# Kernel tuning notes

Measured on AMD Instinct MI355X. Metric: run time of the kernel, lower is better.

The kernel has to match this reference:

```python
import jax, jax.numpy as jnp
import numpy as np

N_IN, M_MID = 512, 256
B, H, W = 16, 64, 64

def setup_inputs() -> dict:
    key = jax.random.key(0)
    ks = jax.random.split(key, 7)
    s = 0.05
    return {
        "x": jax.random.normal(ks[0], (B, N_IN, H, W), dtype=jnp.float32),
        "W_state": jax.random.normal(ks[1], (M_MID, N_IN), dtype=jnp.float32) * s,
        "b_state": jax.random.normal(ks[2], (M_MID,), dtype=jnp.float32) * s,
        "W_proj": jax.random.normal(ks[3], (M_MID, N_IN), dtype=jnp.float32) * s,
        "b_proj": jax.random.normal(ks[4], (M_MID,), dtype=jnp.float32) * s,
        "W_extend": jax.random.normal(ks[5], (N_IN, M_MID), dtype=jnp.float32) * s,
        "b_extend": jax.random.normal(ks[6], (N_IN,), dtype=jnp.float32) * s,
    }

def reference(x, W_state, b_state, W_proj, b_proj, W_extend, b_extend):
    n, c, h, w = x.shape
    hw = h * w
    xf = x.reshape(n, c, hw)                                   # [n, C, HW]
    # 1x1 convs are channel GEMMs over flattened spatial dim
    x_state = jnp.einsum('mc,nch->nmh', W_state, xf) + b_state[None, :, None]   # [n, M, HW]
    x_proj = jnp.einsum('mc,nch->nmh', W_proj, xf) + b_proj[None, :, None]      # [n, M, HW]
    # bmm -> scale -> softmax -> bmm (graph reasoning over M x M)
    scores = jnp.einsum('nmh,nkh->nmk', x_state, x_proj) / jnp.sqrt(jnp.float32(hw))
    attn = jax.nn.softmax(scores, axis=2)                      # [n, M, M]
    x_rstate = jnp.einsum('nmk,nkh->nmh', attn, x_proj)        # [n, M, HW]
    # extend back to C channels + residual
    ext = jnp.einsum('cm,nmh->nch', W_extend, x_rstate) + b_extend[None, :, None]
    return x + ext.reshape(n, c, h, w)
```

## Files before the change

kernel.cpp:

```cpp
#include <hip/hip_runtime.h>
#include <hip/hip_bf16.h>
#include <stdint.h>

typedef __bf16 bf16x8_t __attribute__((ext_vector_type(8)));
typedef float  f32x4_t  __attribute__((ext_vector_type(4)));
typedef short  short8_t __attribute__((ext_vector_type(8)));

__device__ __forceinline__ unsigned short f2b(float f) {
    union { float f; unsigned u; } v; v.f = f;
    unsigned u = v.u;
    return (unsigned short)((u + 0x7FFFu + ((u >> 16) & 1u)) >> 16);
}
__device__ __forceinline__ float b2f(unsigned short b) {
    union { unsigned u; float f; } v; v.u = ((unsigned)b) << 16; return v.f;
}

#define AS3(p) ((__attribute__((address_space(3))) void*)(p))
#define AS1(p) ((const __attribute__((address_space(1))) void*)(p))
#define FENCE() asm volatile("" ::: "memory")

#define NB   16
#define CIN  512
#define MMID 256
#define HW   4096
#define KSPLIT 8
#define ASZ  (128 * 64)

__device__ __forceinline__ void swz3(int gx, int gy, int& bx, int& by, int& bz) {
    const int nwg = gridDim.x, ord = blockIdx.x, q = nwg >> 3;
    const int s = (ord & 7) * q + (ord >> 3);
    by = s % gy;
    const int rem = s / gy;
    bx = rem % gx;
    bz = rem / gx;
}

__global__ __launch_bounds__(256) void prep_weights(
    const float* __restrict__ Ws, const float* __restrict__ Wp,
    const float* __restrict__ Wef, const float* __restrict__ bs,
    const float* __restrict__ bp,
    unsigned short* __restrict__ Wsp, unsigned short* __restrict__ Wex,
    unsigned short* __restrict__ WpT, float* __restrict__ bsp)
{
    int i = blockIdx.x * 256 + threadIdx.x;
    if (i < MMID * CIN) {
        Wsp[i]              = f2b(Ws[i]);
        Wsp[MMID * CIN + i] = f2b(Wp[i]);
        Wex[i]              = f2b(Wef[i]);
        const int c = i >> 8, k = i & (MMID - 1);
        WpT[i] = f2b(Wp[(size_t)k * CIN + c]);
    }
    if (i < MMID) { bsp[i] = bs[i]; bsp[MMID + i] = bp[i]; }
}

__global__ __launch_bounds__(256) void transpose_convert_x(
    const float* __restrict__ x, unsigned short* __restrict__ xT)
{
    __shared__ unsigned short tile[64][66];
    const int n = blockIdx.z, c0 = blockIdx.y * 64, h0 = blockIdx.x * 64;
    const float* s = x + ((size_t)n * CIN + c0) * HW + h0;
    unsigned short* d = xT + ((size_t)n * HW + h0) * CIN + c0;
    const int t = threadIdx.x;
    {
        const int rr = t >> 4, cc = (t & 15) * 4;
        #pragma unroll
        for (int p = 0; p < 4; ++p) {
            int r = p * 16 + rr;
            float4 v = *(const float4*)(s + (size_t)r * HW + cc);
            tile[r][cc + 0] = f2b(v.x); tile[r][cc + 1] = f2b(v.y);
            tile[r][cc + 2] = f2b(v.z); tile[r][cc + 3] = f2b(v.w);
        }
    }
    __syncthreads();
    {
        const int wr = t >> 3, wc = (t & 7) * 8;
        #pragma unroll
        for (int p = 0; p < 2; ++p) {
            int h = p * 32 + wr;
            unsigned short tmp[8];
            #pragma unroll
            for (int j = 0; j < 8; ++j) tmp[j] = tile[wc + j][h];
            *(short8_t*)(d + (size_t)h * CIN + wc) = *(const short8_t*)tmp;
        }
    }
}

__global__ __launch_bounds__(256) void transpose_bf16_64(
    const unsigned short* __restrict__ src, unsigned short* __restrict__ dst,
    int srs, int drs, long long sbs, long long dbs)
{
    __shared__ unsigned short tile[64][66];
    const int n = blockIdx.z, r0 = blockIdx.y * 64, c0 = blockIdx.x * 64;
    const unsigned short* s = src + (size_t)n * sbs + (size_t)r0 * srs + c0;
    unsigned short* d = dst + (size_t)n * dbs + (size_t)c0 * drs + r0;
    const int t = threadIdx.x;
    const int rr = t >> 3, cc = (t & 7) * 8;
    #pragma unroll
    for (int p = 0; p < 2; ++p) {
        int r = p * 32 + rr;
        short8_t v = *(const short8_t*)(s + (size_t)r * srs + cc);
        #pragma unroll
        for (int j = 0; j < 8; ++j) tile[r][cc + j] = ((const unsigned short*)&v)[j];
    }
    __syncthreads();
    #pragma unroll
    for (int p = 0; p < 2; ++p) {
        int c = p * 32 + rr;
        unsigned short tmp[8];
        #pragma unroll
        for (int j = 0; j < 8; ++j) tmp[j] = tile[cc + j][c];
        *(short8_t*)(d + (size_t)c * drs + cc) = *(const short8_t*)tmp;
    }
}

template <int EPI>
__device__ __forceinline__ void epilogue_repack(
    f32x4_t (&acc)[4][4], unsigned short* smem,
    int m0, int n0, int wave, int lane,
    const float* __restrict__ bias, const float* __restrict__ resid,
    void* __restrict__ Cout, int ldc, size_t cbase)
{
    float* fbuf = (float*)smem;
    const int t   = wave * 64 + lane;
    const int l15 = lane & 15, l16 = lane >> 4;
    const int wr2 = wave >> 1;
    const int wc  = (wave & 1) * 64;

    #pragma unroll
    for (int p = 0; p < 4; ++p) {
        __syncthreads();
        if (wr2 == (p >> 1)) {
            const int ihalf = p & 1;
            #pragma unroll
            for (int i2 = 0; i2 < 2; ++i2) {
                const int i = ihalf * 2 + i2;
                #pragma unroll
                for (int r = 0; r < 4; ++r) {
                    const int lrow = i2 * 16 + l16 * 4 + r;
                    #pragma unroll
                    for (int j = 0; j < 4; ++j)
                        fbuf[lrow * 132 + wc + j * 16 + l15] = acc[i][j][r];
                }
            }
        }
        __syncthreads();
        #pragma unroll
        for (int it = 0; it < 2; ++it) {
            const int lrow = it * 16 + (t >> 4);
            const int col  = (t & 15) * 8;
            const int row  = m0 + p * 32 + lrow;
            float v[8];
            *(float4*)&v[0] = *(const float4*)&fbuf[lrow * 132 + col];
            *(float4*)&v[4] = *(const float4*)&fbuf[lrow * 132 + col + 4];
            float badd = 0.f;
            if constexpr (EPI == 0 || EPI == 3) badd = bias[row];
            const size_t idx = cbase + (size_t)row * ldc + n0 + col;
            if constexpr (EPI == 3) {
                float o[8];
                const float* rp = resid + idx;
                float4 r0 = *(const float4*)rp;
                float4 r1 = *(const float4*)(rp + 4);
                o[0] = v[0] + badd + r0.x; o[1] = v[1] + badd + r0.y;
                o[2] = v[2] + badd + r0.z; o[3] = v[3] + badd + r0.w;
                o[4] = v[4] + badd + r1.x; o[5] = v[5] + badd + r1.y;
                o[6] = v[6] + badd + r1.z; o[7] = v[7] + badd + r1.w;
                float* op = (float*)Cout + idx;
                *(float4*)op = *(const float4*)&o[0];
                *(float4*)(op + 4) = *(const float4*)&o[4];
            } else if constexpr (EPI == 1) {
                float* op = (float*)Cout + idx;
                *(float4*)op = *(const float4*)&v[0];
                *(float4*)(op + 4) = *(const float4*)&v[4];
            } else {
                unsigned short o[8];
                #pragma unroll
                for (int k = 0; k < 8; ++k) o[k] = f2b(v[k] + badd);
                *(short8_t*)((unsigned short*)Cout + idx) = *(const short8_t*)o;
            }
        }
    }
}

#define GEMM_KLOOP(Ab, Bb, lda, ldb, KBEG, NT)                                          \
    auto stage = [&](int k0, int b) {                                                   \
        unsigned short* Asb = smem + b * 2 * ASZ;                                       \
        unsigned short* Bsb = Asb + ASZ;                                                \
        _Pragma("unroll")                                                               \
        for (int c = 0; c < 4; ++c) {                                                   \
            const int o   = (c * 256 + t) * 16;                                         \
            const int row = o >> 7;                                                     \
            const int ce  = ((o & 127) ^ ((row & 7) << 4)) >> 1;                        \
            __builtin_amdgcn_global_load_lds(                                           \
                AS1(Ab + (size_t)row * lda + k0 + ce), AS3((char*)Asb + o), 16, 0, 0);  \
            __builtin_amdgcn_global_load_lds(                                           \
                AS1(Bb + (size_t)row * ldb + k0 + ce), AS3((char*)Bsb + o), 16, 0, 0);  \
        }                                                                               \
    };                                                                                  \
    stage(KBEG, 0);                                                                     \
    for (int itk = 0; itk < (NT); ++itk) {                                              \
        const int cur = itk & 1;                                                        \
        if (itk + 1 < (NT)) {                                                           \
            stage(KBEG + (itk + 1) * 64, cur ^ 1);                                      \
            asm volatile("s_waitcnt vmcnt(8)" ::: "memory");                            \
        } else {                                                                        \
            asm volatile("s_waitcnt vmcnt(0)" ::: "memory");                            \
        }                                                                               \
        __builtin_amdgcn_s_barrier();                                                   \
        FENCE();                                                                        \
        const char* Asb = (const char*)(smem + cur * 2 * ASZ);                          \
        const char* Bsb = Asb + 2 * ASZ;                                                \
        const int swz = (l15 & 7) << 4;                                                 \
        _Pragma("unroll")                                                               \
        for (int ks = 0; ks < 2; ++ks) {                                                \
            bf16x8_t af[4], bfr[4];                                                     \
            const int cb = (ks * 64 + l16 * 16) ^ swz;                                  \
            _Pragma("unroll")                                                           \
            for (int i = 0; i < 4; ++i) {                                               \
                af[i]  = *(const bf16x8_t*)(Asb + (wr + i * 16 + l15) * 128 + cb);      \
                bfr[i] = *(const bf16x8_t*)(Bsb + (wc + i * 16 + l15) * 128 + cb);      \
            }                                                                           \
            _Pragma("unroll")                                                           \
            for (int i = 0; i < 4; ++i)                                                 \
                _Pragma("unroll")                                                       \
                for (int j = 0; j < 4; ++j)                                             \
                    acc[i][j] = __builtin_amdgcn_mfma_f32_16x16x32_bf16(                \
                        af[i], bfr[j], acc[i][j], 0, 0, 0);                             \
        }                                                                               \
        FENCE();                                                                        \
        __builtin_amdgcn_s_barrier();                                                   \
        FENCE();                                                                        \
    }

__global__ __launch_bounds__(256) void gemm_conv(
    const unsigned short* __restrict__ Wsp, const unsigned short* __restrict__ xT,
    const float* __restrict__ bsp, unsigned short* __restrict__ Ysp)
{
    __shared__ unsigned short smem[4 * ASZ];

    int bx, by, n;  swz3(HW / 128, CIN / 128, bx, by, n);
    const int m0 = by * 128;
    const int h0 = bx * 128;

    const unsigned short* Ab = Wsp + (size_t)m0 * CIN;
    const unsigned short* Bb = xT + (size_t)n * HW * CIN + (size_t)h0 * CIN;

    const int t    = threadIdx.x;
    const int lane = t & 63;
    const int wave = t >> 6;
    const int wr   = (wave >> 1) * 64;
    const int wc   = (wave & 1) * 64;
    const int l15  = lane & 15;
    const int l16  = lane >> 4;

    f32x4_t acc[4][4] = {};
    GEMM_KLOOP(Ab, Bb, CIN, CIN, 0, CIN / 64)

    epilogue_repack<0>(acc, smem, m0, h0, wave, lane, bsp, nullptr,
                       Ysp, HW, (size_t)n * CIN * HW);
}

__global__ __launch_bounds__(256) void gemm_scores(
    const unsigned short* __restrict__ Ysp, float* __restrict__ scoresP)
{
    __shared__ unsigned short smem[4 * ASZ];

    int bx, by, z;  swz3(MMID / 128, MMID / 128, bx, by, z);
    const int n  = z >> 3;
    const int kc = z & 7;
    const int m0 = by * 128;
    const int n0 = bx * 128;

    const unsigned short* Ab = Ysp + (size_t)n * CIN * HW + (size_t)m0 * HW;
    const unsigned short* Bb = Ysp + (size_t)n * CIN * HW + (size_t)(MMID + n0) * HW;

    const int t    = threadIdx.x;
    const int lane = t & 63;
    const int wave = t >> 6;
    const int wr   = (wave >> 1) * 64;
    const int wc   = (wave & 1) * 64;
    const int l15  = lane & 15;
    const int l16  = lane >> 4;

    f32x4_t acc[4][4] = {};
    const int kbeg = kc * (HW / KSPLIT);
    GEMM_KLOOP(Ab, Bb, HW, HW, kbeg, (HW / KSPLIT) / 64)

    float* outp = scoresP + (size_t)(kc * NB + n) * MMID * MMID;
    epilogue_repack<1>(acc, smem, m0, n0, wave, lane, nullptr, nullptr,
                       outp, MMID, 0);
}

__global__ __launch_bounds__(256) void softmax_rows(
    const float* __restrict__ scoresP, unsigned short* __restrict__ attn)
{
    const int wave = threadIdx.x >> 6;
    const int l    = threadIdx.x & 63;
    const size_t row = (size_t)blockIdx.x * 4 + wave;
    const size_t pstride = (size_t)NB * MMID * MMID;
    float4 v = {0.f, 0.f, 0.f, 0.f};
    #pragma unroll
    for (int p = 0; p < KSPLIT; ++p) {
        float4 u = *(const float4*)(scoresP + p * pstride + row * MMID + l * 4);
        v.x += u.x; v.y += u.y; v.z += u.z; v.w += u.w;
    }
    float mx = fmaxf(fmaxf(v.x, v.y), fmaxf(v.z, v.w));
    #pragma unroll
    for (int off = 32; off; off >>= 1) mx = fmaxf(mx, __shfl_xor(mx, off));
    const float sc = 0.015625f;
    float e0 = __expf((v.x - mx) * sc), e1 = __expf((v.y - mx) * sc);
    float e2 = __expf((v.z - mx) * sc), e3 = __expf((v.w - mx) * sc);
    float sum = e0 + e1 + e2 + e3;
    #pragma unroll
    for (int off = 32; off; off >>= 1) sum += __shfl_xor(sum, off);
    const float inv = 1.0f / sum;
    unsigned short o[4] = { f2b(e0 * inv), f2b(e1 * inv), f2b(e2 * inv), f2b(e3 * inv) };
    *(uint64_t*)(attn + row * MMID + l * 4) = *(const uint64_t*)o;
}

__global__ __launch_bounds__(256) void compute_vec(
    const unsigned short* __restrict__ G, const float* __restrict__ bsp,
    const float* __restrict__ be, float* __restrict__ vec)
{
    const int n = blockIdx.x >> 1;
    const int c = ((blockIdx.x & 1) << 8) + threadIdx.x;
    const unsigned short* g = G + ((size_t)n * CIN + c) * MMID;
    float s = 0.f;
    for (int k = 0; k < MMID; k += 8) {
        short8_t v = *(const short8_t*)(g + k);
        #pragma unroll
        for (int j = 0; j < 8; ++j)
            s += b2f((unsigned short)v[j]) * bsp[MMID + k + j];
    }
    vec[n * CIN + c] = be[c] + s;
}

template <int EPI>
__global__ __launch_bounds__(256) void gemm_nt(
    const unsigned short* __restrict__ A, const unsigned short* __restrict__ B,
    int lda, int ldb, int K,
    long long strideA, long long strideB,
    const float* __restrict__ bias, int bias_bstride,
    const float* __restrict__ resid,
    void* __restrict__ Cout, int ldc, long long strideC,
    int gx, int gy)
{
    __shared__ unsigned short smem[4 * ASZ];

    int bx, by, n;  swz3(gx, gy, bx, by, n);
    const int m0 = by * 128;
    const int n0 = bx * 128;

    const unsigned short* Ab = A + (size_t)n * strideA + (size_t)m0 * lda;
    const unsigned short* Bb = B + (size_t)n * strideB + (size_t)n0 * ldb;

    const int t    = threadIdx.x;
    const int lane = t & 63;
    const int wave = t >> 6;
    const int wr   = (wave >> 1) * 64;
    const int wc   = (wave & 1) * 64;
    const int l15  = lane & 15;
    const int l16  = lane >> 4;

    f32x4_t acc[4][4] = {};
    GEMM_KLOOP(Ab, Bb, lda, ldb, 0, K / 64)

    const float* beff = bias ? bias + (size_t)n * bias_bstride : nullptr;
    epilogue_repack<EPI>(acc, smem, m0, n0, wave, lane, beff, resid,
                         Cout, ldc, (size_t)n * strideC);
}

extern "C" void kernel_launch(void* const* d_in, const int* in_sizes, int n_in,
                              void* d_out, int out_size, void* d_ws, size_t ws_size,
                              hipStream_t stream)
{
    const float* x   = (const float*)d_in[0];
    const float* Ws  = (const float*)d_in[1];
    const float* bs  = (const float*)d_in[2];
    const float* Wp  = (const float*)d_in[3];
    const float* bp  = (const float*)d_in[4];
    const float* Wef = (const float*)d_in[5];
    const float* be  = (const float*)d_in[6];
    float* out = (float*)d_out;

    unsigned short* xT   = (unsigned short*)d_ws;
    unsigned short* Ysp  = xT   + (size_t)NB * HW * CIN;
    unsigned short* Wsp  = Ysp  + (size_t)NB * CIN * HW;
    unsigned short* Wex  = Wsp  + (size_t)CIN * CIN;
    unsigned short* WpT  = Wex  + (size_t)CIN * MMID;
    unsigned short* attn = WpT  + (size_t)CIN * MMID;
    unsigned short* attnT= attn + (size_t)NB * MMID * MMID;
    unsigned short* G    = attnT+ (size_t)NB * MMID * MMID;
    unsigned short* Meff = G    + (size_t)NB * CIN * MMID;
    float* scoresP = (float*)(Meff + (size_t)NB * CIN * CIN);
    float* bsp = scoresP + (size_t)KSPLIT * NB * MMID * MMID;
    float* vec = bsp + CIN;

    prep_weights<<<512, 256, 0, stream>>>(Ws, Wp, Wef, bs, bp, Wsp, Wex, WpT, bsp);

    transpose_convert_x<<<dim3(HW / 64, CIN / 64, NB), 256, 0, stream>>>(x, xT);

    gemm_conv<<<(HW / 128) * (CIN / 128) * NB, 256, 0, stream>>>(
        Wsp, xT, bsp, Ysp);

    gemm_scores<<<(MMID / 128) * (MMID / 128) * NB * KSPLIT, 256, 0, stream>>>(
        Ysp, scoresP);

    softmax_rows<<<NB * MMID / 4, 256, 0, stream>>>(scoresP, attn);

    transpose_bf16_64<<<dim3(MMID / 64, MMID / 64, NB), 256, 0, stream>>>(
        attn, attnT, MMID, MMID, (long long)MMID * MMID, (long long)MMID * MMID);

    gemm_nt<2><<<(MMID / 128) * (CIN / 128) * NB, 256, 0, stream>>>(
        Wex, attnT, MMID, MMID, MMID,
        0LL, (long long)MMID * MMID,
        nullptr, 0, nullptr, G, MMID, (long long)CIN * MMID,
        MMID / 128, CIN / 128);

    compute_vec<<<NB * 2, 256, 0, stream>>>(G, bsp, be, vec);

    gemm_nt<2><<<(CIN / 128) * (CIN / 128) * NB, 256, 0, stream>>>(
        G, WpT, MMID, MMID, MMID,
        (long long)CIN * MMID, 0LL,
        nullptr, 0, nullptr, Meff, CIN, (long long)CIN * CIN,
        CIN / 128, CIN / 128);

    gemm_nt<3><<<(HW / 128) * (CIN / 128) * NB, 256, 0, stream>>>(
        Meff, xT, CIN, CIN, CIN,
        (long long)CIN * CIN, (long long)HW * CIN,
        vec, CIN, x, out, HW, (long long)CIN * HW,
        HW / 128, CIN / 128);
}
```

Baseline: 217.3 us.

## Use 256x256-tile 512-thread GEMM kernel for conv and final extend GEMMs

```diff
diff --git a/kernel.cpp b/kernel.cpp
--- a/kernel.cpp
+++ b/kernel.cpp
@@ -25,6 +25,7 @@
 #define HW   4096
 #define KSPLIT 8
 #define ASZ  (128 * 64)
+#define ASZ2 (256 * 64)
 
 __device__ __forceinline__ void swz3(int gx, int gy, int& bx, int& by, int& bz) {
     const int nwg = gridDim.x, ord = blockIdx.x, q = nwg >> 3;
@@ -231,32 +232,137 @@
         FENCE();                                                                        \
     }
 
-__global__ __launch_bounds__(256) void gemm_conv(
-    const unsigned short* __restrict__ Wsp, const unsigned short* __restrict__ xT,
-    const float* __restrict__ bsp, unsigned short* __restrict__ Ysp)
-{
-    __shared__ unsigned short smem[4 * ASZ];
-
-    int bx, by, n;  swz3(HW / 128, CIN / 128, bx, by, n);
-    const int m0 = by * 128;
-    const int h0 = bx * 128;
-
-    const unsigned short* Ab = Wsp + (size_t)m0 * CIN;
-    const unsigned short* Bb = xT + (size_t)n * HW * CIN + (size_t)h0 * CIN;
+template <int EPI>
+__global__ __launch_bounds__(512, 2) void gemm256(
+    const unsigned short* __restrict__ A, const unsigned short* __restrict__ B,
+    int lda, int ldb, int K,
+    long long strideA, long long strideB,
+    const float* __restrict__ bias, int bias_bstride,
+    const float* __restrict__ resid,
+    void* __restrict__ Cout, int ldc, long long strideC,
+    int gx, int gy)
+{
+    __shared__ unsigned short smem[4 * ASZ2];
+
+    int bx, by, n;  swz3(gx, gy, bx, by, n);
+    const int m0 = by * 256;
+    const int n0 = bx * 256;
+
+    const unsigned short* Ab = A + (size_t)n * strideA + (size_t)m0 * lda;
+    const unsigned short* Bb = B + (size_t)n * strideB + (size_t)n0 * ldb;
 
     const int t    = threadIdx.x;
     const int lane = t & 63;
     const int wave = t >> 6;
-    const int wr   = (wave >> 1) * 64;
-    const int wc   = (wave & 1) * 64;
+    const int wr2  = wave >> 2;
+    const int wc4  = wave & 3;
     const int l15  = lane & 15;
     const int l16  = lane >> 4;
 
-    f32x4_t acc[4][4] = {};
-    GEMM_KLOOP(Ab, Bb, CIN, CIN, 0, CIN / 64)
-
-    epilogue_repack<0>(acc, smem, m0, h0, wave, lane, bsp, nullptr,
-                       Ysp, HW, (size_t)n * CIN * HW);
+    f32x4_t acc[8][4] = {};
+
+    auto stage = [&](int k0, int b) {
+        unsigned short* Asb = smem + b * 2 * ASZ2;
+        unsigned short* Bsb = Asb + ASZ2;
+        #pragma unroll
+        for (int c = 0; c < 4; ++c) {
+            const int o   = (c * 512 + t) * 16;
+            const int row = o >> 7;
+            const int ce  = ((o & 127) ^ ((row & 7) << 4)) >> 1;
+            __builtin_amdgcn_global_load_lds(
+                AS1(Ab + (size_t)row * lda + k0 + ce), AS3((char*)Asb + o), 16, 0, 0);
+            __builtin_amdgcn_global_load_lds(
+                AS1(Bb + (size_t)row * ldb + k0 + ce), AS3((char*)Bsb + o), 16, 0, 0);
+        }
+    };
+
+    const int NT = K / 64;
+    stage(0, 0);
+    for (int itk = 0; itk < NT; ++itk) {
+        const int cur = itk & 1;
+        if (itk + 1 < NT) {
+            stage((itk + 1) * 64, cur ^ 1);
+            asm volatile("s_waitcnt vmcnt(8)" ::: "memory");
+        } else {
+            asm volatile("s_waitcnt vmcnt(0)" ::: "memory");
+        }
+        __builtin_amdgcn_s_barrier();
+        FENCE();
+        const char* Asb = (const char*)(smem + cur * 2 * ASZ2);
+        const char* Bsb = Asb + 2 * ASZ2;
+        const int swz = (l15 & 7) << 4;
+        #pragma unroll
+        for (int ks = 0; ks < 2; ++ks) {
+            const int cb = (ks * 64 + l16 * 16) ^ swz;
+            bf16x8_t af[8], bfr[4];
+            #pragma unroll
+            for (int i = 0; i < 8; ++i)
+                af[i] = *(const bf16x8_t*)(Asb + (wr2 * 128 + i * 16 + l15) * 128 + cb);
+            #pragma unroll
+            for (int j = 0; j < 4; ++j)
+                bfr[j] = *(const bf16x8_t*)(Bsb + (wc4 * 64 + j * 16 + l15) * 128 + cb);
+            #pragma unroll
+            for (int i = 0; i < 8; ++i)
+                #pragma unroll
+                for (int j = 0; j < 4; ++j)
+                    acc[i][j] = __builtin_amdgcn_mfma_f32_16x16x32_bf16(
+                        af[i], bfr[j], acc[i][j], 0, 0, 0);
+        }
+        FENCE();
+        __builtin_amdgcn_s_barrier();
+        FENCE();
+    }
+
+    float* fbuf = (float*)smem;
+    const size_t cbase = (size_t)n * strideC;
+    const float* beff = bias ? bias + (size_t)n * bias_bstride : nullptr;
+    #pragma unroll
+    for (int p = 0; p < 8; ++p) {
+        __syncthreads();
+        if (wr2 == (p >> 2)) {
+            #pragma unroll
+            for (int i2 = 0; i2 < 2; ++i2) {
+                const int i = (p & 3) * 2 + i2;
+                #pragma unroll
+                for (int r = 0; r < 4; ++r) {
+                    const int lrow = i2 * 16 + l16 * 4 + r;
+                    #pragma unroll
+                    for (int j = 0; j < 4; ++j)
+                        fbuf[lrow * 264 + wc4 * 64 + j * 16 + l15] = acc[i][j][r];
+                }
+            }
+        }
+        __syncthreads();
+        #pragma unroll
+        for (int it = 0; it < 2; ++it) {
+            const int lrow = it * 16 + (t >> 5);
+            const int col  = (t & 31) * 8;
+            const int row  = m0 + p * 32 + lrow;
+            float v[8];
+            *(float4*)&v[0] = *(const float4*)&fbuf[lrow * 264 + col];
+            *(float4*)&v[4] = *(const float4*)&fbuf[lrow * 264 + col + 4];
+            const float badd = beff ? beff[row] : 0.f;
+            const size_t idx = cbase + (size_t)row * ldc + n0 + col;
+            if constexpr (EPI == 3) {
+                float o[8];
+                const float* rp = resid + idx;
+                float4 r0 = *(const float4*)rp;
+                float4 r1 = *(const float4*)(rp + 4);
+                o[0] = v[0] + badd + r0.x; o[1] = v[1] + badd + r0.y;
+                o[2] = v[2] + badd + r0.z; o[3] = v[3] + badd + r0.w;
+                o[4] = v[4] + badd + r1.x; o[5] = v[5] + badd + r1.y;
+                o[6] = v[6] + badd + r1.z; o[7] = v[7] + badd + r1.w;
+                float* op = (float*)Cout + idx;
+                *(float4*)op = *(const float4*)&o[0];
+                *(float4*)(op + 4) = *(const float4*)&o[4];
+            } else {
+                unsigned short o[8];
+                #pragma unroll
+                for (int k = 0; k < 8; ++k) o[k] = f2b(v[k] + badd);
+                *(short8_t*)((unsigned short*)Cout + idx) = *(const short8_t*)o;
+            }
+        }
+    }
 }
 
 __global__ __launch_bounds__(256) void gemm_scores(
@@ -399,8 +505,11 @@
 
     transpose_convert_x<<<dim3(HW / 64, CIN / 64, NB), 256, 0, stream>>>(x, xT);
 
-    gemm_conv<<<(HW / 128) * (CIN / 128) * NB, 256, 0, stream>>>(
-        Wsp, xT, bsp, Ysp);
+    gemm256<0><<<(HW / 256) * (CIN / 256) * NB, 512, 0, stream>>>(
+        Wsp, xT, CIN, CIN, CIN,
+        0LL, (long long)HW * CIN,
+        bsp, 0, nullptr, Ysp, HW, (long long)CIN * HW,
+        HW / 256, CIN / 256);
 
     gemm_scores<<<(MMID / 128) * (MMID / 128) * NB * KSPLIT, 256, 0, stream>>>(
         Ysp, scoresP);
@@ -424,9 +533,9 @@
         nullptr, 0, nullptr, Meff, CIN, (long long)CIN * CIN,
         CIN / 128, CIN / 128);
 
-    gemm_nt<3><<<(HW / 128) * (CIN / 128) * NB, 256, 0, stream>>>(
+    gemm256<3><<<(HW / 256) * (CIN / 256) * NB, 512, 0, stream>>>(
         Meff, xT, CIN, CIN, CIN,
         (long long)CIN * CIN, (long long)HW * CIN,
         vec, CIN, x, out, HW, (long long)CIN * HW,
-        HW / 128, CIN / 128);
-}
+        HW / 256, CIN / 256);
+}
```

Result: slower. 224.2 us (+3.2%).
